# Optimization experiments

Measured on AMD Instinct MI355X. Metric: run time of the kernel, lower is better.

Reference implementation:

```python
import jax, jax.numpy as jnp
import numpy as np

N_HEAD = 16
ROPE_THETA = 10000.0


def _rope_cache(T, dim, theta=ROPE_THETA):
    # inv_freq over even indices, as in RotaryEmbedding
    inv_freq = 1.0 / (theta ** (jnp.arange(0, dim, 2, dtype=jnp.float32) / dim))
    freqs = jnp.arange(T, dtype=jnp.float32)[:, None] * inv_freq[None, :]  # [T, dim//2]
    return jnp.cos(freqs), jnp.sin(freqs)


def _apply_rope(x, cos, sin):
    # x: [B, H, T, D]; cos/sin: [T, D//2] broadcast over B,H
    x1 = x[..., ::2]
    x2 = x[..., 1::2]
    # even slots: x1*cos - x2*sin ; odd slots: x2*cos + x1*sin (interleaved rotate-pairs)
    r1 = x1 * cos - x2 * sin
    r2 = x2 * cos + x1 * sin
    return jnp.stack([r1, r2], axis=-1).reshape(x.shape)


def setup_inputs() -> dict:
    key = jax.random.key(0)
    k1, k2, k3 = jax.random.split(key, 3)
    B, T, C = 4, 2048, 1024
    x = jax.random.normal(k1, (B, T, C), dtype=jnp.float32)
    W_qkv = jax.random.normal(k2, (C, 3 * C), dtype=jnp.float32) * (C ** -0.5)
    W_out = jax.random.normal(k3, (C, C), dtype=jnp.float32) * (C ** -0.5)
    return {"x": x, "W_qkv": W_qkv, "W_out": W_out}


def reference(x, W_qkv, W_out):
    B, T, C = x.shape
    H = N_HEAD
    D = C // H
    # fused QKV projection -> [3, B, H, T, D]
    qkv = (x @ W_qkv).reshape(B, T, 3, H, D).transpose(2, 0, 3, 1, 4)
    q, k, v = qkv[0], qkv[1], qkv[2]
    cos, sin = _rope_cache(T, D)
    q = _apply_rope(q, cos, sin)
    k = _apply_rope(k, cos, sin)
    scale = 1.0 / jnp.sqrt(jnp.float32(D))
    scores = jnp.einsum('bhqd,bhkd->bhqk', q, k) * scale  # [B,H,T,T]
    causal_mask = jnp.tril(jnp.ones((T, T), dtype=bool))
    scores = jnp.where(causal_mask, scores, -jnp.inf)
    attn = jax.nn.softmax(scores, axis=-1)
    out = jnp.einsum('bhqk,bhkd->bhqd', attn, v)  # [B,H,T,D]
    out = out.transpose(0, 2, 1, 3).reshape(B, T, C)
    return out @ W_out
```

## Files before the change

### kernel.cpp

```cpp
#include <hip/hip_runtime.h>
#include <hip/hip_bf16.h>
#include <math.h>

#define BATCH 4
#define SEQ   2048
#define CDIM  1024
#define NHEAD 16
#define HDIM  64
#define QKVN  3072
#define QSCALE 0.1803368801111244f

typedef float f32x4 __attribute__((ext_vector_type(4)));
typedef float f32x16 __attribute__((ext_vector_type(16)));
typedef short bf16x8 __attribute__((ext_vector_type(8)));
typedef short bf16x4 __attribute__((ext_vector_type(4)));
typedef int i32x2 __attribute__((ext_vector_type(2)));
typedef int i32x4 __attribute__((ext_vector_type(4)));

static __device__ __forceinline__ unsigned short f2bf(float f) {
    unsigned int u = __float_as_uint(f);
    u += 0x7FFF + ((u >> 16) & 1);
    return (unsigned short)(u >> 16);
}
static __device__ __forceinline__ float bf2f(unsigned short u) {
    return __uint_as_float(((unsigned int)u) << 16);
}
static __device__ __forceinline__ unsigned int pk2bf(float lo, float hi) {
    __hip_bfloat162 h = __float22bfloat162_rn(make_float2(lo, hi));
    return *(unsigned int*)&h;
}
static __device__ __forceinline__ bf16x8 lds_read8(const unsigned short* p) {
    bf16x4 lo = *(const bf16x4*)p;
    bf16x4 hi = *(const bf16x4*)(p + 4);
    return __builtin_shufflevector(lo, hi, 0, 1, 2, 3, 4, 5, 6, 7);
}

static __device__ __forceinline__ void transpose_tile(
    const float* __restrict__ W, unsigned short* __restrict__ Wt,
    int K, int N, int bx, int by, unsigned short (*tile)[65], int tid) {
    const int n0 = bx * 64;
    const int k0 = by * 64;
    const int r = tid >> 4;
    const int c4 = (tid & 15) << 2;
    #pragma unroll
    for (int ii = 0; ii < 4; ii++) {
        int row = r + 16 * ii;
        float4 v = *(const float4*)&W[(size_t)(k0 + row) * N + n0 + c4];
        tile[c4 + 0][row] = f2bf(v.x);
        tile[c4 + 1][row] = f2bf(v.y);
        tile[c4 + 2][row] = f2bf(v.z);
        tile[c4 + 3][row] = f2bf(v.w);
    }
    __syncthreads();
    #pragma unroll
    for (int ii = 0; ii < 4; ii++) {
        int row = r + 16 * ii;
        ushort4 o;
        o.x = tile[row][c4 + 0];
        o.y = tile[row][c4 + 1];
        o.z = tile[row][c4 + 2];
        o.w = tile[row][c4 + 3];
        *(ushort4*)&Wt[(size_t)(n0 + row) * K + k0 + c4] = o;
    }
}

__global__ __launch_bounds__(256) void prep(
    const float* __restrict__ x, const float* __restrict__ W_qkv,
    const float* __restrict__ W_out, float2* __restrict__ ctab,
    unsigned short* __restrict__ xb, unsigned short* __restrict__ wqb,
    unsigned short* __restrict__ wob) {
    __shared__ unsigned short tile[64][65];
    const int blk = blockIdx.x;
    const int tid = threadIdx.x;
    if (blk < 8192) {
        const int i = blk * 256 + tid;
        float4 v = ((const float4*)x)[i];
        ushort4 o;
        o.x = f2bf(v.x); o.y = f2bf(v.y); o.z = f2bf(v.z); o.w = f2bf(v.w);
        ((ushort4*)xb)[i] = o;
    } else if (blk < 8448) {
        const int i = (blk - 8192) * 256 + tid;
        const int dp = i & 31;
        const int t = i >> 5;
        const float invf = powf(10000.0f, -((float)(2 * dp)) / 64.0f);
        float sv, cv;
        __sincosf((float)t * invf, &sv, &cv);
        ctab[i] = make_float2(cv, sv);
    } else if (blk < 9216) {
        const int r = blk - 8448;
        transpose_tile(W_qkv, wqb, CDIM, QKVN, r % 48, r / 48, tile, tid);
    } else {
        const int r = blk - 9216;
        transpose_tile(W_out, wob, CDIM, CDIM, r % 16, r / 16, tile, tid);
    }
}

#define GLDS(gp, lp) __builtin_amdgcn_global_load_lds(                       \
    (const __attribute__((address_space(1))) unsigned int*)(gp),             \
    (__attribute__((address_space(3))) unsigned int*)(lp), 16, 0, 0)

template <typename OUT>
__global__ __launch_bounds__(256, 4) void gemm_bt_bf16(
    const unsigned short* __restrict__ A,
    const unsigned short* __restrict__ Bt,
    OUT* __restrict__ C, int M, int N, int K) {
    __shared__ unsigned short As[128 * 64];
    __shared__ unsigned short Bs[128 * 64];

    const int tid = threadIdx.x;
    const int wave = tid >> 6;
    const int lane = tid & 63;
    const int bm = blockIdx.y * 128;
    const int bn = blockIdx.x * 128;
    const int wm = (wave >> 1) * 64;
    const int wn = (wave & 1) * 64;

    const int sr = tid >> 3;
    const int sc = ((tid & 7) ^ (sr & 7)) << 3;
    const unsigned short* Ag = A + (size_t)(bm + sr) * K + sc;
    const unsigned short* Bg = Bt + (size_t)(bn + sr) * K + sc;
    char* AsW = (char*)As + wave * 1024;
    char* BsW = (char*)Bs + wave * 1024;

    const int fm = lane & 15;
    const int quad = lane >> 4;
    const int sl0 = ((quad ^ (fm & 7)) << 3);
    const int sl1 = (((4 + quad) ^ (fm & 7)) << 3);

    f32x4 acc[4][4];
    #pragma unroll
    for (int i = 0; i < 4; i++)
        #pragma unroll
        for (int j = 0; j < 4; j++)
            acc[i][j] = (f32x4){0.f, 0.f, 0.f, 0.f};

    for (int k0 = 0; k0 < K; k0 += 64) {
        GLDS(Ag + k0, AsW);
        GLDS(Ag + 32 * K + k0, AsW + 4096);
        GLDS(Ag + 64 * K + k0, AsW + 8192);
        GLDS(Ag + 96 * K + k0, AsW + 12288);
        GLDS(Bg + k0, BsW);
        GLDS(Bg + 32 * K + k0, BsW + 4096);
        GLDS(Bg + 64 * K + k0, BsW + 8192);
        GLDS(Bg + 96 * K + k0, BsW + 12288);
        __syncthreads();

        bf16x8 af[4], bfr[4];
        #pragma unroll
        for (int i = 0; i < 4; i++)
            af[i] = *(const bf16x8*)&As[(wm + i * 16 + fm) * 64 + sl0];
        #pragma unroll
        for (int j = 0; j < 4; j++)
            bfr[j] = *(const bf16x8*)&Bs[(wn + j * 16 + fm) * 64 + sl0];
        #pragma unroll
        for (int i = 0; i < 4; i++)
            #pragma unroll
            for (int j = 0; j < 4; j++)
                acc[i][j] = __builtin_amdgcn_mfma_f32_16x16x32_bf16(
                    af[i], bfr[j], acc[i][j], 0, 0, 0);
        #pragma unroll
        for (int i = 0; i < 4; i++)
            af[i] = *(const bf16x8*)&As[(wm + i * 16 + fm) * 64 + sl1];
        #pragma unroll
        for (int j = 0; j < 4; j++)
            bfr[j] = *(const bf16x8*)&Bs[(wn + j * 16 + fm) * 64 + sl1];
        #pragma unroll
        for (int i = 0; i < 4; i++)
            #pragma unroll
            for (int j = 0; j < 4; j++)
                acc[i][j] = __builtin_amdgcn_mfma_f32_16x16x32_bf16(
                    af[i], bfr[j], acc[i][j], 0, 0, 0);
        __syncthreads();
    }

    const int er = quad * 4;
    #pragma unroll
    for (int i = 0; i < 4; i++) {
        #pragma unroll
        for (int j = 0; j < 4; j++) {
            #pragma unroll
            for (int r = 0; r < 4; r++) {
                size_t off = (size_t)(bm + wm + i * 16 + er + r) * N + bn + wn + j * 16 + fm;
                if constexpr (sizeof(OUT) == 2)
                    C[off] = f2bf(acc[i][j][r]);
                else
                    C[off] = acc[i][j][r];
            }
        }
    }
}

__global__ __launch_bounds__(256, 4) void gemm_qkv_fused(
    const unsigned short* __restrict__ A,
    const unsigned short* __restrict__ Bt,
    const float2* __restrict__ ctab,
    unsigned short* __restrict__ Qg,
    unsigned short* __restrict__ Kg,
    unsigned short* __restrict__ Vtg) {
    __shared__ unsigned short SH[16384];
    unsigned short* As = SH;
    unsigned short* Bs = SH + 8192;
    const int K = CDIM;

    const int tid = threadIdx.x;
    const int wave = tid >> 6;
    const int lane = tid & 63;
    const int bm = blockIdx.y * 128;
    const int bn = blockIdx.x * 128;
    const int wm = (wave >> 1) * 64;
    const int wn = (wave & 1) * 64;

    const int sr = tid >> 3;
    const int sc = ((tid & 7) ^ (sr & 7)) << 3;
    const unsigned short* Ag = A + (size_t)(bm + sr) * K + sc;
    const unsigned short* Bg = Bt + (size_t)(bn + sr) * K + sc;
    char* AsW = (char*)SH + wave * 1024;
    char* BsW = (char*)SH + 16384 + wave * 1024;

    const int fm = lane & 15;
    const int quad = lane >> 4;
    const int sl0 = ((quad ^ (fm & 7)) << 3);
    const int sl1 = (((4 + quad) ^ (fm & 7)) << 3);

    f32x4 acc[4][4];
    #pragma unroll
    for (int i = 0; i < 4; i++)
        #pragma unroll
        for (int j = 0; j < 4; j++)
            acc[i][j] = (f32x4){0.f, 0.f, 0.f, 0.f};

    for (int k0 = 0; k0 < K; k0 += 64) {
        GLDS(Ag + k0, AsW);
        GLDS(Ag + 32 * K + k0, AsW + 4096);
        GLDS(Ag + 64 * K + k0, AsW + 8192);
        GLDS(Ag + 96 * K + k0, AsW + 12288);
        GLDS(Bg + k0, BsW);
        GLDS(Bg + 32 * K + k0, BsW + 4096);
        GLDS(Bg + 64 * K + k0, BsW + 8192);
        GLDS(Bg + 96 * K + k0, BsW + 12288);
        __syncthreads();

        bf16x8 af[4], bfr[4];
        #pragma unroll
        for (int i = 0; i < 4; i++)
            af[i] = *(const bf16x8*)&As[(wm + i * 16 + fm) * 64 + sl0];
        #pragma unroll
        for (int j = 0; j < 4; j++)
            bfr[j] = *(const bf16x8*)&Bs[(wn + j * 16 + fm) * 64 + sl0];
        #pragma unroll
        for (int i = 0; i < 4; i++)
            #pragma unroll
            for (int j = 0; j < 4; j++)
                acc[i][j] = __builtin_amdgcn_mfma_f32_16x16x32_bf16(
                    af[i], bfr[j], acc[i][j], 0, 0, 0);
        #pragma unroll
        for (int i = 0; i < 4; i++)
            af[i] = *(const bf16x8*)&As[(wm + i * 16 + fm) * 64 + sl1];
        #pragma unroll
        for (int j = 0; j < 4; j++)
            bfr[j] = *(const bf16x8*)&Bs[(wn + j * 16 + fm) * 64 + sl1];
        #pragma unroll
        for (int i = 0; i < 4; i++)
            #pragma unroll
            for (int j = 0; j < 4; j++)
                acc[i][j] = __builtin_amdgcn_mfma_f32_16x16x32_bf16(
                    af[i], bfr[j], acc[i][j], 0, 0, 0);
        __syncthreads();
    }

    const int s = bn >> 10;
    const int hbase = (bn & 1023) >> 6;
    const int b = bm >> 11;
    const int t0 = bm & 2047;

    #pragma unroll 1
    for (int pass = 0; pass < 2; pass++) {
        if ((wave >> 1) == pass) {
            #pragma unroll
            for (int i = 0; i < 4; i++)
                #pragma unroll
                for (int j = 0; j < 4; j++)
                    #pragma unroll
                    for (int r = 0; r < 4; r++)
                        SH[(i * 16 + quad * 4 + r) * 132 + wn + j * 16 + fm] =
                            f2bf(acc[i][j][r]);
        }
        __syncthreads();

        if (s < 2) {
            unsigned short* dst = (s == 0) ? Qg : Kg;
            const float sc2 = (s == 0) ? QSCALE : 1.0f;
            #pragma unroll
            for (int it = 0; it < 16; it++) {
                const int idx = it * 256 + tid;
                const int row = idx >> 6;
                const int col = (idx & 63) << 1;
                const unsigned int pr = *(const unsigned int*)&SH[row * 132 + col];
                const float x0 = bf2f((unsigned short)pr);
                const float x1 = bf2f((unsigned short)(pr >> 16));
                const int t = t0 + pass * 64 + row;
                const int h = hbase + (col >> 6);
                const int d = col & 63;
                const float2 cs = ctab[t * 32 + (d >> 1)];
                const float r0 = (x0 * cs.x - x1 * cs.y) * sc2;
                const float r1 = (x1 * cs.x + x0 * cs.y) * sc2;
                *(unsigned int*)&dst[((size_t)(b * NHEAD + h) * SEQ + t) * HDIM + d] =
                    pk2bf(r0, r1);
            }
        } else {
            #pragma unroll
            for (int it = 0; it < 8; it++) {
                const int idx = it * 256 + tid;
                const int dcol = idx >> 4;
                const int tq = idx & 15;
                ushort4 o;
                o.x = SH[(tq * 4 + 0) * 132 + dcol];
                o.y = SH[(tq * 4 + 1) * 132 + dcol];
                o.z = SH[(tq * 4 + 2) * 132 + dcol];
                o.w = SH[(tq * 4 + 3) * 132 + dcol];
                const int h = hbase + (dcol >> 6);
                const int dl = dcol & 63;
                const int t = t0 + pass * 64 + tq * 4;
                *(ushort4*)&Vtg[((size_t)(b * NHEAD + h) * HDIM + dl) * SEQ + t] = o;
            }
        }
        __syncthreads();
    }
}

__global__ __launch_bounds__(256, 4) void flash_attn_mfma(
    const unsigned short* __restrict__ Qg,
    const unsigned short* __restrict__ Kg,
    const unsigned short* __restrict__ Vtg,
    unsigned short* __restrict__ att) {
    __shared__ unsigned short Ks[2][64 * 68];
    __shared__ unsigned short Vt[2][64 * 68];

    const int tid = threadIdx.x;
    const int wave = tid >> 6;
    const int lane = tid & 63;
    const int l31 = lane & 31;
    const int hi = lane >> 5;
    const int wq = wave * 32;
    const int bh = blockIdx.x & 63;
    const int qt = 15 - (blockIdx.x >> 6);
    const int b = bh >> 4, h = bh & 15;

    const int r_ld = tid >> 4;
    const int c4 = (tid & 15) << 2;

    const unsigned short* Kbase = Kg + (size_t)bh * SEQ * HDIM;
    const unsigned short* Vbase = Vtg + (size_t)bh * HDIM * SEQ;

    const int qrow = qt * 128 + wq + l31;

    bf16x8 bq[4];
    #pragma unroll
    for (int dc = 0; dc < 4; dc++)
        bq[dc] = *(const bf16x8*)&Qg[((size_t)bh * SEQ + qrow) * HDIM + dc * 16 + hi * 8];

    bf16x8 bones;
    #pragma unroll
    for (int z = 0; z < 8; z++) bones[z] = (short)0x3F80;

    f32x16 O[2], lsum16;
    #pragma unroll
    for (int nt = 0; nt < 2; nt++)
        #pragma unroll
        for (int r = 0; r < 16; r++) O[nt][r] = 0.f;
    #pragma unroll
    for (int r = 0; r < 16; r++) lsum16[r] = 0.f;

    const int jtop = 2 * qt + 1;

    ushort4 kreg[4], vreg[4];
    #pragma unroll
    for (int ii = 0; ii < 4; ii++) {
        const int row = r_ld + 16 * ii;
        kreg[ii] = *(const ushort4*)&Kbase[(size_t)row * HDIM + c4];
        vreg[ii] = *(const ushort4*)&Vbase[(size_t)row * SEQ + c4];
    }
    #pragma unroll
    for (int ii = 0; ii < 4; ii++) {
        const int row = r_ld + 16 * ii;
        *(ushort4*)&Ks[0][row * 68 + c4] = kreg[ii];
        *(ushort4*)&Vt[0][row * 68 + c4] = vreg[ii];
    }
    __syncthreads();

    int cur = 0;
    #pragma unroll 1
    for (int j = 0; j <= jtop; j++) {
        if (j < jtop) {
            #pragma unroll
            for (int ii = 0; ii < 4; ii++) {
                const int row = r_ld + 16 * ii;
                kreg[ii] = *(const ushort4*)&Kbase[(size_t)((j + 1) * 64 + row) * HDIM + c4];
                vreg[ii] = *(const ushort4*)&Vbase[(size_t)row * SEQ + (j + 1) * 64 + c4];
            }
        }

        const bool active = (j * 64) <= (qt * 128 + wq + 31);
        if (active) {
            const unsigned short* Kc = Ks[cur];
            const unsigned short* Vc = Vt[cur];
            const bool diag = (j * 64 + 63) > (qt * 128 + wq);

            #pragma unroll
            for (int kt = 0; kt < 2; kt++) {
                f32x16 sa;
                #pragma unroll
                for (int r = 0; r < 16; r++) sa[r] = 0.f;
                __builtin_amdgcn_s_setprio(1);
                #pragma unroll
                for (int dc = 0; dc < 4; dc++) {
                    bf16x8 ak = lds_read8(&Kc[(kt * 32 + l31) * 68 + dc * 16 + hi * 8]);
                    sa = __builtin_amdgcn_mfma_f32_32x32x16_bf16(ak, bq[dc], sa, 0, 0, 0);
                }
                __builtin_amdgcn_s_setprio(0);

                if (diag) {
                    const int kb = j * 64 + kt * 32 + 4 * hi;
                    #pragma unroll
                    for (int r = 0; r < 16; r++) {
                        const int kg = kb + (r & 3) + 8 * (r >> 2);
                        if (kg > qrow) sa[r] = -INFINITY;
                    }
                }

                unsigned int p32[8];
                #pragma unroll
                for (int v = 0; v < 8; v++)
                    p32[v] = pk2bf(exp2f(sa[2 * v]), exp2f(sa[2 * v + 1]));

                #pragma unroll
                for (int c = 0; c < 2; c++) {
                    i32x2 s0 = __builtin_amdgcn_permlane32_swap(
                        (int)p32[4 * c + 0], (int)p32[4 * c + 2], false, false);
                    i32x2 s1 = __builtin_amdgcn_permlane32_swap(
                        (int)p32[4 * c + 1], (int)p32[4 * c + 3], false, false);
                    i32x4 pw = (i32x4){s0[0], s1[0], s0[1], s1[1]};
                    bf16x8 pa = *(bf16x8*)&pw;
                    __builtin_amdgcn_s_setprio(1);
                    lsum16 = __builtin_amdgcn_mfma_f32_32x32x16_bf16(pa, bones, lsum16, 0, 0, 0);
                    #pragma unroll
                    for (int nt = 0; nt < 2; nt++) {
                        bf16x8 bv = lds_read8(&Vc[(nt * 32 + l31) * 68 + kt * 32 + c * 16 + hi * 8]);
                        O[nt] = __builtin_amdgcn_mfma_f32_32x32x16_bf16(pa, bv, O[nt], 0, 0, 0);
                    }
                    __builtin_amdgcn_s_setprio(0);
                }
            }
        }

        if (j < jtop) {
            const int nb = cur ^ 1;
            #pragma unroll
            for (int ii = 0; ii < 4; ii++) {
                const int row = r_ld + 16 * ii;
                *(ushort4*)&Ks[nb][row * 68 + c4] = kreg[ii];
                *(ushort4*)&Vt[nb][row * 68 + c4] = vreg[ii];
            }
        }

        __syncthreads();
        cur ^= 1;
    }

    #pragma unroll
    for (int r = 0; r < 16; r++) {
        const float inv = 1.0f / lsum16[r];
        const int qloc = (r & 3) + 8 * (r >> 2) + 4 * hi;
        const int row = qt * 128 + wq + qloc;
        #pragma unroll
        for (int nt = 0; nt < 2; nt++)
            att[(size_t)(b * SEQ + row) * CDIM + h * HDIM + nt * 32 + l31] =
                f2bf(O[nt][r] * inv);
    }
}

extern "C" void kernel_launch(void* const* d_in, const int* in_sizes, int n_in,
                              void* d_out, int out_size, void* d_ws, size_t ws_size,
                              hipStream_t stream) {
    const float* x     = (const float*)d_in[0];
    const float* W_qkv = (const float*)d_in[1];
    const float* W_out = (const float*)d_in[2];
    float* out = (float*)d_out;

    const int M = BATCH * SEQ;

    float2* ctab = (float2*)d_ws;
    unsigned short* xb   = (unsigned short*)(ctab + SEQ * 32);
    unsigned short* wqb  = xb + (size_t)M * CDIM;
    unsigned short* wob  = wqb + (size_t)CDIM * QKVN;
    unsigned short* attb = wob + (size_t)CDIM * CDIM;
    unsigned short* Qg   = attb + (size_t)M * CDIM;
    unsigned short* Kg   = Qg + (size_t)M * CDIM;
    unsigned short* Vtg  = Kg + (size_t)M * CDIM;

    prep<<<9472, 256, 0, stream>>>(x, W_qkv, W_out, ctab, xb, wqb, wob);

    gemm_qkv_fused<<<dim3(QKVN / 128, M / 128), 256, 0, stream>>>(
        xb, wqb, ctab, Qg, Kg, Vtg);

    flash_attn_mfma<<<BATCH * NHEAD * (SEQ / 128), 256, 0, stream>>>(Qg, Kg, Vtg, attb);

    gemm_bt_bf16<float><<<dim3(CDIM / 128, M / 128), 256, 0, stream>>>(
        attb, wob, out, M, CDIM, CDIM);
}
```

Baseline: 262.0 us.

## Load K/V tiles directly into swizzled LDS with global-to-LDS loads

The flash attention kernel now copies K and V tiles straight from global memory into LDS with the GLDS direct-load path. This replaces the old staging through registers and separate LDS stores. The padded 68-wide LDS rows become unpadded 64-wide rows with an XOR swizzle on 16-byte chunks, so each MFMA operand fetch is a single 128-bit LDS read without bank conflicts. This frees VGPRs and removes LDS write instructions from the loop. It depends on GLDS being defined elsewhere and on correct vmcnt waiting before the barrier.

```diff
diff --git a/kernel.cpp b/kernel.cpp
--- a/kernel.cpp
+++ b/kernel.cpp
@@ -28,11 +28,6 @@
 static __device__ __forceinline__ unsigned int pk2bf(float lo, float hi) {
     __hip_bfloat162 h = __float22bfloat162_rn(make_float2(lo, hi));
     return *(unsigned int*)&h;
-}
-static __device__ __forceinline__ bf16x8 lds_read8(const unsigned short* p) {
-    bf16x4 lo = *(const bf16x4*)p;
-    bf16x4 hi = *(const bf16x4*)(p + 4);
-    return __builtin_shufflevector(lo, hi, 0, 1, 2, 3, 4, 5, 6, 7);
 }
 
 static __device__ __forceinline__ void transpose_tile(
@@ -333,8 +328,8 @@
     const unsigned short* __restrict__ Kg,
     const unsigned short* __restrict__ Vtg,
     unsigned short* __restrict__ att) {
-    __shared__ unsigned short Ks[2][64 * 68];
-    __shared__ unsigned short Vt[2][64 * 68];
+    __shared__ unsigned short Ks[2][64 * 64];
+    __shared__ unsigned short Vt[2][64 * 64];
 
     const int tid = threadIdx.x;
     const int wave = tid >> 6;
@@ -346,13 +341,13 @@
     const int qt = 15 - (blockIdx.x >> 6);
     const int b = bh >> 4, h = bh & 15;
 
-    const int r_ld = tid >> 4;
-    const int c4 = (tid & 15) << 2;
-
-    const unsigned short* Kbase = Kg + (size_t)bh * SEQ * HDIM;
-    const unsigned short* Vbase = Vtg + (size_t)bh * HDIM * SEQ;
+    const int srow = tid >> 3;
+    const int scg = ((tid & 7) ^ (srow & 7)) << 3;
+    const unsigned short* Ksrc = Kg + (size_t)bh * SEQ * HDIM + (size_t)srow * HDIM + scg;
+    const unsigned short* Vsrc = Vtg + (size_t)bh * HDIM * SEQ + (size_t)srow * SEQ + scg;
 
     const int qrow = qt * 128 + wq + l31;
+    const int x7 = (l31 & 7);
 
     bf16x8 bq[4];
     #pragma unroll
@@ -373,18 +368,11 @@
 
     const int jtop = 2 * qt + 1;
 
-    ushort4 kreg[4], vreg[4];
-    #pragma unroll
-    for (int ii = 0; ii < 4; ii++) {
-        const int row = r_ld + 16 * ii;
-        kreg[ii] = *(const ushort4*)&Kbase[(size_t)row * HDIM + c4];
-        vreg[ii] = *(const ushort4*)&Vbase[(size_t)row * SEQ + c4];
-    }
-    #pragma unroll
-    for (int ii = 0; ii < 4; ii++) {
-        const int row = r_ld + 16 * ii;
-        *(ushort4*)&Ks[0][row * 68 + c4] = kreg[ii];
-        *(ushort4*)&Vt[0][row * 68 + c4] = vreg[ii];
+    {
+        char* kb = (char*)Ks[0] + wave * 1024;
+        char* vb = (char*)Vt[0] + wave * 1024;
+        GLDS(Ksrc, kb);                 GLDS(Ksrc + 32 * HDIM, kb + 4096);
+        GLDS(Vsrc, vb);                 GLDS(Vsrc + 32 * SEQ, vb + 4096);
     }
     __syncthreads();
 
@@ -392,12 +380,12 @@
     #pragma unroll 1
     for (int j = 0; j <= jtop; j++) {
         if (j < jtop) {
-            #pragma unroll
-            for (int ii = 0; ii < 4; ii++) {
-                const int row = r_ld + 16 * ii;
-                kreg[ii] = *(const ushort4*)&Kbase[(size_t)((j + 1) * 64 + row) * HDIM + c4];
-                vreg[ii] = *(const ushort4*)&Vbase[(size_t)row * SEQ + (j + 1) * 64 + c4];
-            }
+            char* kb = (char*)Ks[cur ^ 1] + wave * 1024;
+            char* vb = (char*)Vt[cur ^ 1] + wave * 1024;
+            const unsigned short* kjs = Ksrc + (size_t)(j + 1) * 64 * HDIM;
+            const unsigned short* vjs = Vsrc + (j + 1) * 64;
+            GLDS(kjs, kb);              GLDS(kjs + 32 * HDIM, kb + 4096);
+            GLDS(vjs, vb);              GLDS(vjs + 32 * SEQ, vb + 4096);
         }
 
         const bool active = (j * 64) <= (qt * 128 + wq + 31);
@@ -414,7 +402,8 @@
                 __builtin_amdgcn_s_setprio(1);
                 #pragma unroll
                 for (int dc = 0; dc < 4; dc++) {
-                    bf16x8 ak = lds_read8(&Kc[(kt * 32 + l31) * 68 + dc * 16 + hi * 8]);
+                    bf16x8 ak = *(const bf16x8*)&Kc[(kt * 32 + l31) * 64 +
+                                                    (((dc * 2 + hi) ^ x7) << 3)];
                     sa = __builtin_amdgcn_mfma_f32_32x32x16_bf16(ak, bq[dc], sa, 0, 0, 0);
                 }
                 __builtin_amdgcn_s_setprio(0);
@@ -445,21 +434,12 @@
                     lsum16 = __builtin_amdgcn_mfma_f32_32x32x16_bf16(pa, bones, lsum16, 0, 0, 0);
                     #pragma unroll
                     for (int nt = 0; nt < 2; nt++) {
-                        bf16x8 bv = lds_read8(&Vc[(nt * 32 + l31) * 68 + kt * 32 + c * 16 + hi * 8]);
+                        bf16x8 bv = *(const bf16x8*)&Vc[(nt * 32 + l31) * 64 +
+                                                        (((kt * 4 + c * 2 + hi) ^ x7) << 3)];
                         O[nt] = __builtin_amdgcn_mfma_f32_32x32x16_bf16(pa, bv, O[nt], 0, 0, 0);
                     }
                     __builtin_amdgcn_s_setprio(0);
                 }
-            }
-        }
-
-        if (j < jtop) {
-            const int nb = cur ^ 1;
-            #pragma unroll
-            for (int ii = 0; ii < 4; ii++) {
-                const int row = r_ld + 16 * ii;
-                *(ushort4*)&Ks[nb][row * 68 + c4] = kreg[ii];
-                *(ushort4*)&Vt[nb][row * 68 + c4] = vreg[ii];
             }
         }
 
```

After: 265.7 us. About the same (+1.4%).
